# Optimization experiments

Hardware: AMD Instinct MI355X
Metric: run time of the kernel (lower is better)

Reference implementation:

```python
import jax, jax.numpy as jnp
import numpy as np

B, T, E, H = 4, 1024, 1024, 16
F = E // H  # head_feature = 64
EPS = 1e-5


def setup_inputs() -> dict:
    key = jax.random.key(0)
    ks = jax.random.split(key, 7)
    return {
        "x": jax.random.normal(ks[0], (B, T, E), dtype=jnp.float32),
        "q_w": jax.random.normal(ks[1], (H, E, F), dtype=jnp.float32),
        "k_w": jax.random.normal(ks[2], (H, E, F), dtype=jnp.float32),
        "v_w": jax.random.normal(ks[3], (H, E, F), dtype=jnp.float32),
        "fr_w": jax.random.normal(ks[4], (B, E, E), dtype=jnp.float32),
        "ff_w": jax.random.normal(ks[5], (E, E), dtype=jnp.float32),
        "ff_b": jax.random.normal(ks[6], (E,), dtype=jnp.float32),
        "ln1_w": jnp.ones((T, E), dtype=jnp.float32),
        "ln1_b": jnp.zeros((T, E), dtype=jnp.float32),
        "ln2_w": jnp.ones((T, E), dtype=jnp.float32),
        "ln2_b": jnp.zeros((T, E), dtype=jnp.float32),
    }


def _layernorm_2d(x, w, b):
    # LayerNorm over the last TWO dims ([T, E]), matching nn.LayerNorm([T, E])
    mean = jnp.mean(x, axis=(-2, -1), keepdims=True)
    var = jnp.mean(jnp.square(x - mean), axis=(-2, -1), keepdims=True)
    return (x - mean) * jax.lax.rsqrt(var + EPS) * w + b


def _attention(x, q_w, k_w, v_w, fr_w):
    # projections: [B,T,E] x [H,E,F] -> [B,H,T,F]
    q = jnp.einsum("bte,hef->bhtf", x, q_w)
    k = jnp.einsum("bte,hef->bhtf", x, k_w)
    v = jnp.einsum("bte,hef->bhtf", x, v_w)
    scores = jnp.einsum("bhqf,bhkf->bhqk", q, k)  # [B,H,T,T]
    # faithful to source: multiplicative mask (-1e9 on strict upper tri, +1 added everywhere)
    ones = jnp.ones((T, T), dtype=scores.dtype)
    mask = -1.0e9 * jnp.triu(ones, k=1) + ones
    scores = scores * mask
    attn = jax.nn.softmax(scores / jnp.sqrt(jnp.float32(F)), axis=-1)
    z = jnp.einsum("bhqk,bhkf->bhqf", attn, v)  # [B,H,T,F]
    z = z.transpose(0, 2, 1, 3).reshape(B, T, E)  # merge heads
    return jnp.einsum("bte,bed->btd", z, fr_w)  # per-batch feature reduction


def reference(x, q_w, k_w, v_w, fr_w, ff_w, ff_b, ln1_w, ln1_b, ln2_w, ln2_b):
    z = _attention(x, q_w, k_w, v_w, fr_w)
    z1 = _layernorm_2d(x + z, ln1_w, ln1_b)
    z2 = jax.nn.relu(jnp.einsum("bte,de->btd", z1, ff_w) + ff_b)
    return _layernorm_2d(z1 + z2, ln2_w, ln2_b)
```

## Files before the change

### kernel.cpp

```cpp
#include <hip/hip_runtime.h>
#include <math.h>

constexpr int Bc = 4, Tc = 1024, Ec = 1024, Hc = 16, Fc = 64;

typedef __attribute__((ext_vector_type(8))) short bf16x8;
typedef __attribute__((ext_vector_type(4))) float f32x4;

__device__ __forceinline__ ushort f2bf(float x) {
  union { float f; unsigned u; } v; v.f = x;
  unsigned r = v.u + 0x7fffu + ((v.u >> 16) & 1u);
  return (ushort)(r >> 16);
}
__device__ __forceinline__ float bf2f(ushort h) {
  union { float f; unsigned u; } v; v.u = ((unsigned)h) << 16; return v.f;
}
__device__ __forceinline__ void split3(float x, ushort& h, ushort& m, ushort& l) {
  h = f2bf(x);
  float r1 = x - bf2f(h);
  m = f2bf(r1);
  float r2 = r1 - bf2f(m);
  l = f2bf(r2);
}
__device__ __forceinline__ void split2(float x, ushort& h, ushort& l) {
  h = f2bf(x);
  l = f2bf(x - bf2f(h));
}
__device__ __forceinline__ void split3t(float x, ushort& h, ushort& m, ushort& l) {
  union { float f; unsigned u; } v; v.f = x;
  h = (ushort)(v.u >> 16);
  union { float f; unsigned u; } hf; hf.u = v.u & 0xffff0000u;
  float r1 = x - hf.f;
  union { float f; unsigned u; } v1; v1.f = r1;
  m = (ushort)(v1.u >> 16);
  union { float f; unsigned u; } mf; mf.u = v1.u & 0xffff0000u;
  float r2 = r1 - mf.f;
  union { float f; unsigned u; } v2; v2.f = r2;
  l = (ushort)(v2.u >> 16);
}

#define FRAG_IDX(tile, quad, l) (((((tile) * 4) + (quad)) * 16 + (l)) * 8)

__global__ __launch_bounds__(256) void x_split(
    const float* __restrict__ x, ushort* __restrict__ xh,
    ushort* __restrict__ xm, ushort* __restrict__ xl)
{
  const int i = blockIdx.x * 256 + threadIdx.x;
  const float4 a = ((const float4*)x)[i * 2];
  const float4 b = ((const float4*)x)[i * 2 + 1];
  const float xs[8] = {a.x, a.y, a.z, a.w, b.x, b.y, b.z, b.w};
  bf16x8 h, m, l;
#pragma unroll
  for (int j = 0; j < 8; ++j) {
    ushort hu, mu, lu;
    split3t(xs[j], hu, mu, lu);
    h[j] = (short)hu; m[j] = (short)mu; l[j] = (short)lu;
  }
  ((bf16x8*)xh)[i] = h;
  ((bf16x8*)xm)[i] = m;
  ((bf16x8*)xl)[i] = l;
}

__global__ __launch_bounds__(256) void transp_w(
    const float* __restrict__ qw, const float* __restrict__ kw,
    const float* __restrict__ vw, ushort* __restrict__ wT)
{
  const int zi = blockIdx.z;
  const float* src = (zi == 0) ? qw : (zi == 1) ? kw : vw;
  ushort* dst = wT + (size_t)(zi * 3) * (1u << 20);
  const int ns = (zi == 2) ? 1 : 3;
  const int h = blockIdx.y, e0 = blockIdx.x * 64;
  __shared__ float T[64][68];
  const int tid = threadIdx.x;
  {
    const int er = tid >> 4, fr = (tid & 15) * 4;
#pragma unroll
    for (int i = 0; i < 4; ++i) {
      const float4 v = *(const float4*)&src[((size_t)(h * 1024 + e0 + er + i * 16)) * 64 + fr];
      *(float4*)&T[er + i * 16][fr] = v;
    }
  }
  __syncthreads();
  const int f = tid >> 2, eo = (tid & 3) * 16;
  ushort hs[16], ms[16], ls[16];
#pragma unroll
  for (int j = 0; j < 16; ++j) split3(T[eo + j][f], hs[j], ms[j], ls[j]);
  const size_t nbase = (size_t)(h * 64 + f) * 1024 + e0 + eo;
  bf16x8 v0, v1;
#pragma unroll
  for (int j = 0; j < 8; ++j) { v0[j] = (short)hs[j]; v1[j] = (short)hs[j + 8]; }
  *(bf16x8*)&dst[nbase] = v0; *(bf16x8*)&dst[nbase + 8] = v1;
  if (ns == 3) {
#pragma unroll
    for (int j = 0; j < 8; ++j) { v0[j] = (short)ms[j]; v1[j] = (short)ms[j + 8]; }
    *(bf16x8*)&dst[(1u << 20) + nbase] = v0; *(bf16x8*)&dst[(1u << 20) + nbase + 8] = v1;
#pragma unroll
    for (int j = 0; j < 8; ++j) { v0[j] = (short)ls[j]; v1[j] = (short)ls[j + 8]; }
    *(bf16x8*)&dst[(2u << 20) + nbase] = v0; *(bf16x8*)&dst[(2u << 20) + nbase + 8] = v1;
  }
}

__global__ __launch_bounds__(256) void transp_frw(
    const float* __restrict__ frw, ushort* __restrict__ frT)
{
  const int bb = blockIdx.z;
  const int e0 = blockIdx.x * 64, d0 = blockIdx.y * 64;
  __shared__ float T[64][68];
  const int tid = threadIdx.x;
  {
    const int er = tid >> 4, dr = (tid & 15) * 4;
#pragma unroll
    for (int i = 0; i < 4; ++i) {
      const float4 v = *(const float4*)&frw[((size_t)bb * 1024 + e0 + er + i * 16) * 1024 + d0 + dr];
      *(float4*)&T[er + i * 16][dr] = v;
    }
  }
  __syncthreads();
  const int d = tid >> 2, eo = (tid & 3) * 16;
  ushort hs[16], ls[16];
#pragma unroll
  for (int j = 0; j < 16; ++j) split2(T[eo + j][d], hs[j], ls[j]);
  const size_t nbase = ((size_t)bb * 1024 + d0 + d) * 1024 + e0 + eo;
  bf16x8 v0, v1;
#pragma unroll
  for (int j = 0; j < 8; ++j) { v0[j] = (short)hs[j]; v1[j] = (short)hs[j + 8]; }
  *(bf16x8*)&frT[nbase] = v0; *(bf16x8*)&frT[nbase + 8] = v1;
#pragma unroll
  for (int j = 0; j < 8; ++j) { v0[j] = (short)ls[j]; v1[j] = (short)ls[j + 8]; }
  *(bf16x8*)&frT[(4u << 20) + nbase] = v0; *(bf16x8*)&frT[(4u << 20) + nbase + 8] = v1;
}

__global__ __launch_bounds__(256) void proj_all_ps(
    const ushort* __restrict__ xh, const ushort* __restrict__ xm,
    const ushort* __restrict__ xl, const ushort* __restrict__ wT,
    float* __restrict__ qf, ushort* __restrict__ kh,
    ushort* __restrict__ km, ushort* __restrict__ kl,
    ushort* __restrict__ vt)
{
  const int zi = blockIdx.z;
  const int m0 = blockIdx.x * 128, n0 = blockIdx.y * 128;
  __shared__ ushort As[3 * 4096];
  __shared__ ushort Bs[3 * 4096];
  const int tid = threadIdx.x;
  const int wave = tid >> 6, lane = tid & 63, l15 = lane & 15, quad = lane >> 4;
  const int wm = wave >> 1, wn = wave & 1;
  const int sr = tid >> 1, q0 = (tid & 1) * 2;
  const int wb0 = FRAG_IDX(sr >> 4, q0, sr & 15);
  const int wb1 = FRAG_IDX(sr >> 4, q0 + 1, sr & 15);
  f32x4 acc[4][4] = {};

  const size_t arow = (size_t)(m0 + sr) * 1024 + q0 * 8;
  const ushort* axh = xh + arow;
  const ushort* axm = xm + arow;
  const ushort* axl = xl + arow;

  if (zi < 2) {
    const ushort* wt = wT + (size_t)zi * 3 * (1u << 20);
    const ushort* bpb = wt + (size_t)(n0 + sr) * 1024 + q0 * 8;
    bf16x8 pah0 = *(const bf16x8*)(axh);
    bf16x8 pah1 = *(const bf16x8*)(axh + 8);
    bf16x8 pam0 = *(const bf16x8*)(axm);
    bf16x8 pam1 = *(const bf16x8*)(axm + 8);
    bf16x8 pal0 = *(const bf16x8*)(axl);
    bf16x8 pal1 = *(const bf16x8*)(axl + 8);
    bf16x8 pb0[3], pb1[3];
#pragma unroll
    for (int s = 0; s < 3; ++s) {
      const ushort* bp = bpb + ((size_t)s << 20);
      pb0[s] = *(const bf16x8*)(bp);
      pb1[s] = *(const bf16x8*)(bp + 8);
    }
    for (int k0 = 0; k0 < 1024; k0 += 32) {
      __syncthreads();
      {
        *(bf16x8*)&As[wb0] = pah0;        *(bf16x8*)&As[wb1] = pah1;
        *(bf16x8*)&As[4096 + wb0] = pam0; *(bf16x8*)&As[4096 + wb1] = pam1;
        *(bf16x8*)&As[8192 + wb0] = pal0; *(bf16x8*)&As[8192 + wb1] = pal1;
#pragma unroll
        for (int s = 0; s < 3; ++s) {
          *(bf16x8*)&Bs[s * 4096 + wb0] = pb0[s];
          *(bf16x8*)&Bs[s * 4096 + wb1] = pb1[s];
        }
      }
      __syncthreads();
      if (k0 < 992) {
        const int ko = k0 + 32;
        pah0 = *(const bf16x8*)(axh + ko);
        pah1 = *(const bf16x8*)(axh + ko + 8);
        pam0 = *(const bf16x8*)(axm + ko);
        pam1 = *(const bf16x8*)(axm + ko + 8);
        pal0 = *(const bf16x8*)(axl + ko);
        pal1 = *(const bf16x8*)(axl + ko + 8);
#pragma unroll
        for (int s = 0; s < 3; ++s) {
          const ushort* bp = bpb + ((size_t)s << 20) + ko;
          pb0[s] = *(const bf16x8*)(bp);
          pb1[s] = *(const bf16x8*)(bp + 8);
        }
      }
      bf16x8 af[4][3];
#pragma unroll
      for (int tm = 0; tm < 4; ++tm)
#pragma unroll
        for (int s = 0; s < 3; ++s)
          af[tm][s] = *(const bf16x8*)&As[s * 4096 + FRAG_IDX(wm * 4 + tm, quad, l15)];
#pragma unroll
      for (int tn = 0; tn < 4; ++tn) {
        const int bi = FRAG_IDX(wn * 4 + tn, quad, l15);
        bf16x8 b0 = *(const bf16x8*)&Bs[bi];
        bf16x8 b1 = *(const bf16x8*)&Bs[4096 + bi];
        bf16x8 b2 = *(const bf16x8*)&Bs[8192 + bi];
#pragma unroll
        for (int tm = 0; tm < 4; ++tm) {
          f32x4 a = acc[tm][tn];
          a = __builtin_amdgcn_mfma_f32_16x16x32_bf16(af[tm][0], b0, a, 0, 0, 0);
          a = __builtin_amdgcn_mfma_f32_16x16x32_bf16(af[tm][0], b1, a, 0, 0, 0);
          a = __builtin_amdgcn_mfma_f32_16x16x32_bf16(af[tm][1], b0, a, 0, 0, 0);
          a = __builtin_amdgcn_mfma_f32_16x16x32_bf16(af[tm][0], b2, a, 0, 0, 0);
          a = __builtin_amdgcn_mfma_f32_16x16x32_bf16(af[tm][1], b1, a, 0, 0, 0);
          a = __builtin_amdgcn_mfma_f32_16x16x32_bf16(af[tm][2], b0, a, 0, 0, 0);
          acc[tm][tn] = a;
        }
      }
    }
#pragma unroll
    for (int tm = 0; tm < 4; ++tm) {
#pragma unroll
      for (int tn = 0; tn < 4; ++tn) {
#pragma unroll
        for (int r = 0; r < 4; ++r) {
          int m = m0 + wm * 64 + tm * 16 + quad * 4 + r;
          int n = n0 + wn * 64 + tn * 16 + l15;
          int b = m >> 10, t = m & 1023, h = n >> 6, f = n & 63;
          size_t idx = (((size_t)(b * 16 + h)) * 1024 + t) * 64 + f;
          if (zi == 0) {
            qf[idx] = acc[tm][tn][r];
          } else {
            ushort hu, mu, lu;
            split3(acc[tm][tn][r], hu, mu, lu);
            kh[idx] = hu; km[idx] = mu; kl[idx] = lu;
          }
        }
      }
    }
  } else {
    const ushort* wt = wT + (size_t)6 * (1u << 20);
    const ushort* bpb = wt + (size_t)(n0 + sr) * 1024 + q0 * 8;
    bf16x8 pah0 = *(const bf16x8*)(axh);
    bf16x8 pah1 = *(const bf16x8*)(axh + 8);
    bf16x8 pb0 = *(const bf16x8*)(bpb);
    bf16x8 pb1 = *(const bf16x8*)(bpb + 8);
    for (int k0 = 0; k0 < 1024; k0 += 32) {
      __syncthreads();
      {
        *(bf16x8*)&As[wb0] = pah0; *(bf16x8*)&As[wb1] = pah1;
        *(bf16x8*)&Bs[wb0] = pb0;  *(bf16x8*)&Bs[wb1] = pb1;
      }
      __syncthreads();
      if (k0 < 992) {
        const int ko = k0 + 32;
        pah0 = *(const bf16x8*)(axh + ko);
        pah1 = *(const bf16x8*)(axh + ko + 8);
        pb0 = *(const bf16x8*)(bpb + ko);
        pb1 = *(const bf16x8*)(bpb + ko + 8);
      }
      bf16x8 af[4];
#pragma unroll
      for (int tm = 0; tm < 4; ++tm)
        af[tm] = *(const bf16x8*)&As[FRAG_IDX(wm * 4 + tm, quad, l15)];
#pragma unroll
      for (int tn = 0; tn < 4; ++tn) {
        bf16x8 b0 = *(const bf16x8*)&Bs[FRAG_IDX(wn * 4 + tn, quad, l15)];
#pragma unroll
        for (int tm = 0; tm < 4; ++tm)
          acc[tm][tn] = __builtin_amdgcn_mfma_f32_16x16x32_bf16(af[tm], b0, acc[tm][tn], 0, 0, 0);
      }
    }
#pragma unroll
    for (int tm = 0; tm < 4; ++tm) {
#pragma unroll
      for (int tn = 0; tn < 4; ++tn) {
#pragma unroll
        for (int r = 0; r < 4; ++r) {
          int m = m0 + wm * 64 + tm * 16 + quad * 4 + r;
          int n = n0 + wn * 64 + tn * 16 + l15;
          int b = m >> 10, t = m & 1023, h = n >> 6, f = n & 63;
          vt[(((size_t)(b * 16 + h)) * 64 + f) * 1024 + t] = f2bf(acc[tm][tn][r]);
        }
      }
    }
  }
}

__global__ __launch_bounds__(256) void proj_all_mfma(
    const float* __restrict__ x, const ushort* __restrict__ wT,
    float* __restrict__ qf, ushort* __restrict__ kh,
    ushort* __restrict__ km, ushort* __restrict__ kl,
    ushort* __restrict__ vt)
{
  const int zi = blockIdx.z;
  const int m0 = blockIdx.x * 128, n0 = blockIdx.y * 128;
  __shared__ ushort As[3 * 4096];
  __shared__ ushort Bs[3 * 4096];
  const int tid = threadIdx.x;
  const int wave = tid >> 6, lane = tid & 63, l15 = lane & 15, quad = lane >> 4;
  const int wm = wave >> 1, wn = wave & 1;
  const int sr = tid >> 1, q0 = (tid & 1) * 2;
  const int wb0 = FRAG_IDX(sr >> 4, q0, sr & 15);
  const int wb1 = FRAG_IDX(sr >> 4, q0 + 1, sr & 15);
  f32x4 acc[4][4] = {};

  const float* apx = x + (size_t)(m0 + sr) * 1024 + q0 * 8;
  float4 px0 = *(const float4*)(apx);
  float4 px1 = *(const float4*)(apx + 4);
  float4 px2 = *(const float4*)(apx + 8);
  float4 px3 = *(const float4*)(apx + 12);

  if (zi < 2) {
    const ushort* wt = wT + (size_t)zi * 3 * (1u << 20);
    const ushort* bpb = wt + (size_t)(n0 + sr) * 1024 + q0 * 8;
    bf16x8 pb0[3], pb1[3];
#pragma unroll
    for (int s = 0; s < 3; ++s) {
      const ushort* bp = bpb + ((size_t)s << 20);
      pb0[s] = *(const bf16x8*)(bp);
      pb1[s] = *(const bf16x8*)(bp + 8);
    }
    for (int k0 = 0; k0 < 1024; k0 += 32) {
      __syncthreads();
      {
        float xs[16];
        *(float4*)&xs[0]  = px0;
        *(float4*)&xs[4]  = px1;
        *(float4*)&xs[8]  = px2;
        *(float4*)&xs[12] = px3;
        bf16x8 h0, h1, m0v, m1v, l0, l1;
#pragma unroll
        for (int j = 0; j < 8; ++j) {
          ushort hu, mu, lu;
          split3t(xs[j], hu, mu, lu);
          h0[j] = (short)hu; m0v[j] = (short)mu; l0[j] = (short)lu;
          split3t(xs[j + 8], hu, mu, lu);
          h1[j] = (short)hu; m1v[j] = (short)mu; l1[j] = (short)lu;
        }
        *(bf16x8*)&As[wb0] = h0;          *(bf16x8*)&As[wb1] = h1;
        *(bf16x8*)&As[4096 + wb0] = m0v;  *(bf16x8*)&As[4096 + wb1] = m1v;
        *(bf16x8*)&As[8192 + wb0] = l0;   *(bf16x8*)&As[8192 + wb1] = l1;
#pragma unroll
        for (int s = 0; s < 3; ++s) {
          *(bf16x8*)&Bs[s * 4096 + wb0] = pb0[s];
          *(bf16x8*)&Bs[s * 4096 + wb1] = pb1[s];
        }
      }
      __syncthreads();
      if (k0 < 992) {
        const float* nx = apx + k0 + 32;
        px0 = *(const float4*)(nx);
        px1 = *(const float4*)(nx + 4);
        px2 = *(const float4*)(nx + 8);
        px3 = *(const float4*)(nx + 12);
#pragma unroll
        for (int s = 0; s < 3; ++s) {
          const ushort* bp = bpb + ((size_t)s << 20) + k0 + 32;
          pb0[s] = *(const bf16x8*)(bp);
          pb1[s] = *(const bf16x8*)(bp + 8);
        }
      }
      bf16x8 af[4][3];
#pragma unroll
      for (int tm = 0; tm < 4; ++tm)
#pragma unroll
        for (int s = 0; s < 3; ++s)
          af[tm][s] = *(const bf16x8*)&As[s * 4096 + FRAG_IDX(wm * 4 + tm, quad, l15)];
#pragma unroll
      for (int tn = 0; tn < 4; ++tn) {
        const int bi = FRAG_IDX(wn * 4 + tn, quad, l15);
        bf16x8 b0 = *(const bf16x8*)&Bs[bi];
        bf16x8 b1 = *(const bf16x8*)&Bs[4096 + bi];
        bf16x8 b2 = *(const bf16x8*)&Bs[8192 + bi];
#pragma unroll
        for (int tm = 0; tm < 4; ++tm) {
          f32x4 a = acc[tm][tn];
          a = __builtin_amdgcn_mfma_f32_16x16x32_bf16(af[tm][0], b0, a, 0, 0, 0);
          a = __builtin_amdgcn_mfma_f32_16x16x32_bf16(af[tm][0], b1, a, 0, 0, 0);
          a = __builtin_amdgcn_mfma_f32_16x16x32_bf16(af[tm][1], b0, a, 0, 0, 0);
          a = __builtin_amdgcn_mfma_f32_16x16x32_bf16(af[tm][0], b2, a, 0, 0, 0);
          a = __builtin_amdgcn_mfma_f32_16x16x32_bf16(af[tm][1], b1, a, 0, 0, 0);
          a = __builtin_amdgcn_mfma_f32_16x16x32_bf16(af[tm][2], b0, a, 0, 0, 0);
          acc[tm][tn] = a;
        }
      }
    }
#pragma unroll
    for (int tm = 0; tm < 4; ++tm) {
#pragma unroll
      for (int tn = 0; tn < 4; ++tn) {
#pragma unroll
        for (int r = 0; r < 4; ++r) {
          int m = m0 + wm * 64 + tm * 16 + quad * 4 + r;
          int n = n0 + wn * 64 + tn * 16 + l15;
          int b = m >> 10, t = m & 1023, h = n >> 6, f = n & 63;
          size_t idx = (((size_t)(b * 16 + h)) * 1024 + t) * 64 + f;
          if (zi == 0) {
            qf[idx] = acc[tm][tn][r];
          } else {
            ushort hu, mu, lu;
            split3(acc[tm][tn][r], hu, mu, lu);
            kh[idx] = hu; km[idx] = mu; kl[idx] = lu;
          }
        }
      }
    }
  } else {
    const ushort* wt = wT + (size_t)6 * (1u << 20);
    const ushort* bpb = wt + (size_t)(n0 + sr) * 1024 + q0 * 8;
    bf16x8 pb0 = *(const bf16x8*)(bpb);
    bf16x8 pb1 = *(const bf16x8*)(bpb + 8);
    for (int k0 = 0; k0 < 1024; k0 += 32) {
      __syncthreads();
      {
        float xs[16];
        *(float4*)&xs[0]  = px0;
        *(float4*)&xs[4]  = px1;
        *(float4*)&xs[8]  = px2;
        *(float4*)&xs[12] = px3;
        bf16x8 h0, h1;
#pragma unroll
        for (int j = 0; j < 8; ++j) {
          h0[j] = (short)f2bf(xs[j]);
          h1[j] = (short)f2bf(xs[j + 8]);
        }
        *(bf16x8*)&As[wb0] = h0; *(bf16x8*)&As[wb1] = h1;
        *(bf16x8*)&Bs[wb0] = pb0; *(bf16x8*)&Bs[wb1] = pb1;
      }
      __syncthreads();
      if (k0 < 992) {
        const float* nx = apx + k0 + 32;
        px0 = *(const float4*)(nx);
        px1 = *(const float4*)(nx + 4);
        px2 = *(const float4*)(nx + 8);
        px3 = *(const float4*)(nx + 12);
        pb0 = *(const bf16x8*)(bpb + k0 + 32);
        pb1 = *(const bf16x8*)(bpb + k0 + 40);
      }
      bf16x8 af[4];
#pragma unroll
      for (int tm = 0; tm < 4; ++tm)
        af[tm] = *(const bf16x8*)&As[FRAG_IDX(wm * 4 + tm, quad, l15)];
#pragma unroll
      for (int tn = 0; tn < 4; ++tn) {
        bf16x8 b0 = *(const bf16x8*)&Bs[FRAG_IDX(wn * 4 + tn, quad, l15)];
#pragma unroll
        for (int tm = 0; tm < 4; ++tm)
          acc[tm][tn] = __builtin_amdgcn_mfma_f32_16x16x32_bf16(af[tm], b0, acc[tm][tn], 0, 0, 0);
      }
    }
#pragma unroll
    for (int tm = 0; tm < 4; ++tm) {
#pragma unroll
      for (int tn = 0; tn < 4; ++tn) {
#pragma unroll
        for (int r = 0; r < 4; ++r) {
          int m = m0 + wm * 64 + tm * 16 + quad * 4 + r;
          int n = n0 + wn * 64 + tn * 16 + l15;
          int b = m >> 10, t = m & 1023, h = n >> 6, f = n & 63;
          vt[(((size_t)(b * 16 + h)) * 64 + f) * 1024 + t] = f2bf(acc[tm][tn][r]);
        }
      }
    }
  }
}

__global__ __launch_bounds__(512) void attn_mfma(
    const float* __restrict__ qf, const ushort* __restrict__ kh,
    const ushort* __restrict__ km, const ushort* __restrict__ kl,
    const ushort* __restrict__ vt, ushort* __restrict__ zh, ushort* __restrict__ zl)
{
  __shared__ ushort Ks[3][64][68];
  __shared__ ushort Vs[64][68];
  __shared__ ushort Pl[8][16][68];

  const int tid = threadIdx.x;
  const int wave = tid >> 6, lane = tid & 63;
  const int l15 = lane & 15, quad = lane >> 4;
  const int bh = blockIdx.y;
  const int qbase = blockIdx.x * 128;

  bf16x8 aqh[2], aqm[2], aql[2];
  {
    const int qrow = qbase + wave * 16 + l15;
    const float* qp = qf + ((size_t)bh * Tc + qrow) * Fc;
#pragma unroll
    for (int ks = 0; ks < 2; ++ks) {
      int f0 = ks * 32 + quad * 8;
      float4 x0 = *(const float4*)(qp + f0);
      float4 x1 = *(const float4*)(qp + f0 + 4);
      float xs[8] = {x0.x, x0.y, x0.z, x0.w, x1.x, x1.y, x1.z, x1.w};
#pragma unroll
      for (int j = 0; j < 8; ++j) {
        ushort hu, mu, lu;
        split3(xs[j], hu, mu, lu);
        aqh[ks][j] = (short)hu; aqm[ks][j] = (short)mu; aql[ks][j] = (short)lu;
      }
    }
  }

  f32x4 o[4] = {{0,0,0,0},{0,0,0,0},{0,0,0,0},{0,0,0,0}};
  float m_run[4], l_run[4];
#pragma unroll
  for (int r = 0; r < 4; ++r) { m_run[r] = -1e30f; l_run[r] = 0.f; }

  const int srow = tid >> 3, sc8 = tid & 7;
  const size_t kbase = (size_t)bh * Tc * Fc;
  const size_t vbase = (size_t)bh * Fc * Tc;
  const ushort* kp0 = kh + kbase + (size_t)srow * Fc + sc8 * 8;
  const ushort* kp1 = km + kbase + (size_t)srow * Fc + sc8 * 8;
  const ushort* kp2 = kl + kbase + (size_t)srow * Fc + sc8 * 8;
  const ushort* vp  = vt + vbase + (size_t)srow * Tc + sc8 * 8;

  for (int kt = 0; kt < Tc; kt += 64) {
    __syncthreads();
    {
      const size_t ko = (size_t)kt * Fc;
      *(bf16x8*)&Ks[0][srow][sc8 * 8] = *(const bf16x8*)(kp0 + ko);
      *(bf16x8*)&Ks[1][srow][sc8 * 8] = *(const bf16x8*)(kp1 + ko);
      *(bf16x8*)&Ks[2][srow][sc8 * 8] = *(const bf16x8*)(kp2 + ko);
      *(bf16x8*)&Vs[srow][sc8 * 8]    = *(const bf16x8*)(vp + kt);
    }
    __syncthreads();

    f32x4 sacc[4] = {{0,0,0,0},{0,0,0,0},{0,0,0,0},{0,0,0,0}};
#pragma unroll
    for (int nt = 0; nt < 4; ++nt) {
      int key = nt * 16 + l15;
#pragma unroll
      for (int ks = 0; ks < 2; ++ks) {
        int f0 = ks * 32 + quad * 8;
        bf16x8 bh_ = *(const bf16x8*)&Ks[0][key][f0];
        bf16x8 bm_ = *(const bf16x8*)&Ks[1][key][f0];
        bf16x8 bl_ = *(const bf16x8*)&Ks[2][key][f0];
        sacc[nt] = __builtin_amdgcn_mfma_f32_16x16x32_bf16(aqh[ks], bh_, sacc[nt], 0, 0, 0);
        sacc[nt] = __builtin_amdgcn_mfma_f32_16x16x32_bf16(aqh[ks], bm_, sacc[nt], 0, 0, 0);
        sacc[nt] = __builtin_amdgcn_mfma_f32_16x16x32_bf16(aqm[ks], bh_, sacc[nt], 0, 0, 0);
        sacc[nt] = __builtin_amdgcn_mfma_f32_16x16x32_bf16(aqh[ks], bl_, sacc[nt], 0, 0, 0);
        sacc[nt] = __builtin_amdgcn_mfma_f32_16x16x32_bf16(aqm[ks], bm_, sacc[nt], 0, 0, 0);
        sacc[nt] = __builtin_amdgcn_mfma_f32_16x16x32_bf16(aql[ks], bh_, sacc[nt], 0, 0, 0);
      }
    }

    const int rowg0 = qbase + wave * 16 + quad * 4;
    float mx[4];
#pragma unroll
    for (int r = 0; r < 4; ++r) mx[r] = -1e30f;
#pragma unroll
    for (int nt = 0; nt < 4; ++nt) {
      int key = kt + nt * 16 + l15;
#pragma unroll
      for (int r = 0; r < 4; ++r) {
        float s = sacc[nt][r];
        if (key > rowg0 + r) s *= -1.0e9f + 1.0f;
        s *= 0.125f;
        sacc[nt][r] = s;
        mx[r] = fmaxf(mx[r], s);
      }
    }
#pragma unroll
    for (int r = 0; r < 4; ++r)
#pragma unroll
      for (int d = 1; d < 16; d <<= 1) mx[r] = fmaxf(mx[r], __shfl_xor(mx[r], d));

    float corr[4], ps[4];
#pragma unroll
    for (int r = 0; r < 4; ++r) {
      float m2 = fmaxf(m_run[r], mx[r]);
      corr[r] = __expf(m_run[r] - m2);
      m_run[r] = m2;
      ps[r] = 0.f;
    }
#pragma unroll
    for (int nt = 0; nt < 4; ++nt) {
#pragma unroll
      for (int r = 0; r < 4; ++r) {
        float p = __expf(sacc[nt][r] - m_run[r]);
        ps[r] += p;
        Pl[wave][quad * 4 + r][nt * 16 + l15] = f2bf(p);
      }
    }
#pragma unroll
    for (int r = 0; r < 4; ++r) {
#pragma unroll
      for (int d = 1; d < 16; d <<= 1) ps[r] += __shfl_xor(ps[r], d);
      l_run[r] = l_run[r] * corr[r] + ps[r];
#pragma unroll
      for (int ft = 0; ft < 4; ++ft) o[ft][r] *= corr[r];
    }

#pragma unroll
    for (int ks2 = 0; ks2 < 2; ++ks2) {
      bf16x8 pa = *(const bf16x8*)&Pl[wave][l15][ks2 * 32 + quad * 8];
#pragma unroll
      for (int ft = 0; ft < 4; ++ft) {
        bf16x8 vb = *(const bf16x8*)&Vs[ft * 16 + l15][ks2 * 32 + quad * 8];
        o[ft] = __builtin_amdgcn_mfma_f32_16x16x32_bf16(pa, vb, o[ft], 0, 0, 0);
      }
    }
  }

  const int b = bh >> 4, h = bh & 15;
#pragma unroll
  for (int r = 0; r < 4; ++r) {
    float inv = 1.f / l_run[r];
    int row = qbase + wave * 16 + quad * 4 + r;
    size_t base = ((size_t)(b * Tc + row)) * Ec + h * Fc;
#pragma unroll
    for (int ft = 0; ft < 4; ++ft) {
      ushort hu, lu;
      split2(o[ft][r] * inv, hu, lu);
      zh[base + ft * 16 + l15] = hu;
      zl[base + ft * 16 + l15] = lu;
    }
  }
}

__global__ __launch_bounds__(256) void gemm_fr_mfma(
    const ushort* __restrict__ zh, const ushort* __restrict__ zl,
    const ushort* __restrict__ frT, const float* __restrict__ x,
    float* __restrict__ s1, float2* __restrict__ part)
{
  const int bb = blockIdx.z;
  const int m0 = blockIdx.x * 128, n0 = blockIdx.y * 64;
  __shared__ ushort Ah[4096], Al[4096], Bh[2048], Bl[2048];
  __shared__ float2 red[256];
  const int tid = threadIdx.x;
  const int wave = tid >> 6, lane = tid & 63, l15 = lane & 15, quad = lane >> 4;
  const int wm = wave >> 1, wn = wave & 1;
  const int sr = tid >> 1, q0 = (tid & 1) * 2;
  const int wb0 = FRAG_IDX(sr >> 4, q0, sr & 15);
  const int wb1 = FRAG_IDX(sr >> 4, q0 + 1, sr & 15);
  const int sr2 = tid >> 2, qb = tid & 3;
  const int wbB = FRAG_IDX(sr2 >> 4, qb, sr2 & 15);
  f32x4 acc[4][2] = {};
  const size_t abase = ((size_t)bb * 1024 + m0 + sr) * 1024 + q0 * 8;
  const size_t bbase = ((size_t)bb * 1024 + n0 + sr2) * 1024 + qb * 8;
  const ushort* blp = frT + (4u << 20);
  bf16x8 pAh0 = *(const bf16x8*)(zh + abase);
  bf16x8 pAh1 = *(const bf16x8*)(zh + abase + 8);
  bf16x8 pAl0 = *(const bf16x8*)(zl + abase);
  bf16x8 pAl1 = *(const bf16x8*)(zl + abase + 8);
  bf16x8 pBh  = *(const bf16x8*)(frT + bbase);
  bf16x8 pBl  = *(const bf16x8*)(blp + bbase);
  for (int k0 = 0; k0 < 1024; k0 += 32) {
    __syncthreads();
    {
      *(bf16x8*)&Ah[wb0] = pAh0;
      *(bf16x8*)&Ah[wb1] = pAh1;
      *(bf16x8*)&Al[wb0] = pAl0;
      *(bf16x8*)&Al[wb1] = pAl1;
      *(bf16x8*)&Bh[wbB] = pBh;
      *(bf16x8*)&Bl[wbB] = pBl;
    }
    __syncthreads();
    if (k0 < 992) {
      pAh0 = *(const bf16x8*)(zh + abase + k0 + 32);
      pAh1 = *(const bf16x8*)(zh + abase + k0 + 40);
      pAl0 = *(const bf16x8*)(zl + abase + k0 + 32);
      pAl1 = *(const bf16x8*)(zl + abase + k0 + 40);
      pBh  = *(const bf16x8*)(frT + bbase + k0 + 32);
      pBl  = *(const bf16x8*)(blp + bbase + k0 + 32);
    }
    bf16x8 ah[4], al[4];
#pragma unroll
    for (int tm = 0; tm < 4; ++tm) {
      ah[tm] = *(const bf16x8*)&Ah[FRAG_IDX(wm * 4 + tm, quad, l15)];
      al[tm] = *(const bf16x8*)&Al[FRAG_IDX(wm * 4 + tm, quad, l15)];
    }
#pragma unroll
    for (int tn = 0; tn < 2; ++tn) {
      const int bi = FRAG_IDX(wn * 2 + tn, quad, l15);
      bf16x8 b0 = *(const bf16x8*)&Bh[bi];
      bf16x8 b1 = *(const bf16x8*)&Bl[bi];
#pragma unroll
      for (int tm = 0; tm < 4; ++tm) {
        f32x4 a = acc[tm][tn];
        a = __builtin_amdgcn_mfma_f32_16x16x32_bf16(ah[tm], b0, a, 0, 0, 0);
        a = __builtin_amdgcn_mfma_f32_16x16x32_bf16(ah[tm], b1, a, 0, 0, 0);
        a = __builtin_amdgcn_mfma_f32_16x16x32_bf16(al[tm], b0, a, 0, 0, 0);
        acc[tm][tn] = a;
      }
    }
  }
  float sum = 0.f, sq = 0.f;
#pragma unroll
  for (int tm = 0; tm < 4; ++tm) {
#pragma unroll
    for (int tn = 0; tn < 2; ++tn) {
#pragma unroll
      for (int r = 0; r < 4; ++r) {
        int m = m0 + wm * 64 + tm * 16 + quad * 4 + r;
        int n = n0 + wn * 32 + tn * 16 + l15;
        size_t idx = ((size_t)bb * 1024 + m) * 1024 + n;
        float o = x[idx] + acc[tm][tn][r];
        s1[idx] = o;
        sum += o; sq += o * o;
      }
    }
  }
  red[tid] = make_float2(sum, sq);
  __syncthreads();
  for (int s = 128; s > 0; s >>= 1) {
    if (tid < s) { red[tid].x += red[tid + s].x; red[tid].y += red[tid + s].y; }
    __syncthreads();
  }
  if (tid == 0) part[bb * 128 + blockIdx.x * 16 + blockIdx.y] = red[0];
}

__global__ __launch_bounds__(256) void gemm_ff_mfma(
    const ushort* __restrict__ z1h, const ushort* __restrict__ z1l,
    const ushort* __restrict__ fwh, const ushort* __restrict__ fwl,
    const float* __restrict__ ffb, float* __restrict__ s2,
    float2* __restrict__ part)
{
  const int m0 = blockIdx.x * 128, n0 = blockIdx.y * 64;
  __shared__ ushort Ah[4096], Al[4096], Bh[2048], Bl[2048];
  __shared__ float2 red[256];
  const int tid = threadIdx.x;
  const int wave = tid >> 6, lane = tid & 63, l15 = lane & 15, quad = lane >> 4;
  const int wm = wave >> 1, wn = wave & 1;
  const int sr = tid >> 1, q0 = (tid & 1) * 2;
  const int wb0 = FRAG_IDX(sr >> 4, q0, sr & 15);
  const int wb1 = FRAG_IDX(sr >> 4, q0 + 1, sr & 15);
  const int sr2 = tid >> 2, qb = tid & 3;
  const int wbB = FRAG_IDX(sr2 >> 4, qb, sr2 & 15);
  f32x4 acc[4][2] = {};
  const size_t abase = (size_t)(m0 + sr) * 1024 + q0 * 8;
  const size_t bbase = (size_t)(n0 + sr2) * 1024 + qb * 8;
  bf16x8 pAh0 = *(const bf16x8*)(z1h + abase);
  bf16x8 pAh1 = *(const bf16x8*)(z1h + abase + 8);
  bf16x8 pAl0 = *(const bf16x8*)(z1l + abase);
  bf16x8 pAl1 = *(const bf16x8*)(z1l + abase + 8);
  bf16x8 pBh  = *(const bf16x8*)(fwh + bbase);
  bf16x8 pBl  = *(const bf16x8*)(fwl + bbase);
  for (int k0 = 0; k0 < 1024; k0 += 32) {
    __syncthreads();
    {
      *(bf16x8*)&Ah[wb0] = pAh0;
      *(bf16x8*)&Ah[wb1] = pAh1;
      *(bf16x8*)&Al[wb0] = pAl0;
      *(bf16x8*)&Al[wb1] = pAl1;
      *(bf16x8*)&Bh[wbB] = pBh;
      *(bf16x8*)&Bl[wbB] = pBl;
    }
    __syncthreads();
    if (k0 < 992) {
      pAh0 = *(const bf16x8*)(z1h + abase + k0 + 32);
      pAh1 = *(const bf16x8*)(z1h + abase + k0 + 40);
      pAl0 = *(const bf16x8*)(z1l + abase + k0 + 32);
      pAl1 = *(const bf16x8*)(z1l + abase + k0 + 40);
      pBh  = *(const bf16x8*)(fwh + bbase + k0 + 32);
      pBl  = *(const bf16x8*)(fwl + bbase + k0 + 32);
    }
    bf16x8 ah[4], al[4];
#pragma unroll
    for (int tm = 0; tm < 4; ++tm) {
      ah[tm] = *(const bf16x8*)&Ah[FRAG_IDX(wm * 4 + tm, quad, l15)];
      al[tm] = *(const bf16x8*)&Al[FRAG_IDX(wm * 4 + tm, quad, l15)];
    }
#pragma unroll
    for (int tn = 0; tn < 2; ++tn) {
      const int bi = FRAG_IDX(wn * 2 + tn, quad, l15);
      bf16x8 b0 = *(const bf16x8*)&Bh[bi];
      bf16x8 b1 = *(const bf16x8*)&Bl[bi];
#pragma unroll
      for (int tm = 0; tm < 4; ++tm) {
        f32x4 a = acc[tm][tn];
        a = __builtin_amdgcn_mfma_f32_16x16x32_bf16(ah[tm], b0, a, 0, 0, 0);
        a = __builtin_amdgcn_mfma_f32_16x16x32_bf16(ah[tm], b1, a, 0, 0, 0);
        a = __builtin_amdgcn_mfma_f32_16x16x32_bf16(al[tm], b0, a, 0, 0, 0);
        acc[tm][tn] = a;
      }
    }
  }
  float sum = 0.f, sq = 0.f;
#pragma unroll
  for (int tm = 0; tm < 4; ++tm) {
#pragma unroll
    for (int tn = 0; tn < 2; ++tn) {
#pragma unroll
      for (int r = 0; r < 4; ++r) {
        int m = m0 + wm * 64 + tm * 16 + quad * 4 + r;
        int n = n0 + wn * 32 + tn * 16 + l15;
        size_t idx = (size_t)m * 1024 + n;
        float z1v = bf2f(z1h[idx]) + bf2f(z1l[idx]);
        float o = z1v + fmaxf(acc[tm][tn][r] + ffb[n], 0.f);
        s2[idx] = o;
        sum += o; sq += o * o;
      }
    }
  }
  red[tid] = make_float2(sum, sq);
  __syncthreads();
  for (int s = 128; s > 0; s >>= 1) {
    if (tid < s) { red[tid].x += red[tid + s].x; red[tid].y += red[tid + s].y; }
    __syncthreads();
  }
  if (tid == 0) part[blockIdx.x * 16 + blockIdx.y] = red[0];
}

__global__ __launch_bounds__(256) void ln_stats(
    const float2* __restrict__ part, float2* __restrict__ stats, int npart)
{
  __shared__ double sd[256], sq[256];
  const int tid = threadIdx.x;
  double as = 0.0, aq = 0.0;
  for (int i = tid; i < npart; i += 256) {
    float2 p = part[blockIdx.x * npart + i];
    as += (double)p.x; aq += (double)p.y;
  }
  sd[tid] = as; sq[tid] = aq;
  __syncthreads();
  for (int s = 128; s > 0; s >>= 1) {
    if (tid < s) { sd[tid] += sd[tid + s]; sq[tid] += sq[tid + s]; }
    __syncthreads();
  }
  if (tid == 0) {
    const double n = (double)Tc * Ec;
    double mean = sd[0] / n;
    double var = sq[0] / n - mean * mean;
    if (var < 0.0) var = 0.0;
    double rs = 1.0 / sqrt(var + 1e-5);
    stats[blockIdx.x] = make_float2((float)mean, (float)rs);
  }
}

__global__ __launch_bounds__(256) void ln_norm_split(
    const float* __restrict__ s, const float2* __restrict__ stats,
    const float* __restrict__ w, const float* __restrict__ bias,
    ushort* __restrict__ oh, ushort* __restrict__ ol,
    const float* __restrict__ ffw, ushort* __restrict__ fwh, ushort* __restrict__ fwl)
{
  if (blockIdx.x >= 4096) {
    int i = (blockIdx.x - 4096) * 256 + threadIdx.x;
#pragma unroll
    for (int j = 0; j < 4; ++j) {
      int idx = i * 4 + j;
      float4 v = ((const float4*)ffw)[idx];
      ushort4 h, l;
      split2(v.x, h.x, l.x); split2(v.y, h.y, l.y);
      split2(v.z, h.z, l.z); split2(v.w, h.w, l.w);
      ((ushort4*)fwh)[idx] = h; ((ushort4*)fwl)[idx] = l;
    }
    return;
  }
  int i = blockIdx.x * 256 + threadIdx.x;
  int b = i >> 18;
  int te4 = i & ((1 << 18) - 1);
  float2 st = stats[b];
  float4 sv = ((const float4*)s)[i];
  float4 wv = ((const float4*)w)[te4];
  float4 bv = ((const float4*)bias)[te4];
  float4 o;
  o.x = (sv.x - st.x) * st.y * wv.x + bv.x;
  o.y = (sv.y - st.x) * st.y * wv.y + bv.y;
  o.z = (sv.z - st.x) * st.y * wv.z + bv.z;
  o.w = (sv.w - st.x) * st.y * wv.w + bv.w;
  ushort4 h, l;
  split2(o.x, h.x, l.x); split2(o.y, h.y, l.y);
  split2(o.z, h.z, l.z); split2(o.w, h.w, l.w);
  ((ushort4*)oh)[i] = h; ((ushort4*)ol)[i] = l;
}

__global__ __launch_bounds__(256) void ln_norm(
    const float* __restrict__ s, const float2* __restrict__ stats,
    const float* __restrict__ w, const float* __restrict__ bias,
    float* __restrict__ out)
{
  int i = blockIdx.x * 256 + threadIdx.x;
  if (i >= (Bc * Tc * Ec) / 4) return;
  int b = i >> 18;
  int te4 = i & ((1 << 18) - 1);
  float2 st = stats[b];
  float4 sv = ((const float4*)s)[i];
  float4 wv = ((const float4*)w)[te4];
  float4 bv = ((const float4*)bias)[te4];
  float4 o;
  o.x = (sv.x - st.x) * st.y * wv.x + bv.x;
  o.y = (sv.y - st.x) * st.y * wv.y + bv.y;
  o.z = (sv.z - st.x) * st.y * wv.z + bv.z;
  o.w = (sv.w - st.x) * st.y * wv.w + bv.w;
  ((float4*)out)[i] = o;
}

extern "C" void kernel_launch(void* const* d_in, const int* in_sizes, int n_in,
                              void* d_out, int out_size, void* d_ws, size_t ws_size,
                              hipStream_t stream)
{
  const float* x    = (const float*)d_in[0];
  const float* qw   = (const float*)d_in[1];
  const float* kw   = (const float*)d_in[2];
  const float* vw   = (const float*)d_in[3];
  const float* frw  = (const float*)d_in[4];
  const float* ffw  = (const float*)d_in[5];
  const float* ffb  = (const float*)d_in[6];
  const float* ln1w = (const float*)d_in[7];
  const float* ln1b = (const float*)d_in[8];
  const float* ln2w = (const float*)d_in[9];
  const float* ln2b = (const float*)d_in[10];
  float* out = (float*)d_out;
  char* W = (char*)d_ws;

  const size_t MB = 1ull << 20;
  float*  qf  = (float*)(W);
  ushort* kh  = (ushort*)(W + 16 * MB);
  ushort* km  = (ushort*)(W + 24 * MB);
  ushort* kl  = (ushort*)(W + 32 * MB);
  ushort* vt  = (ushort*)(W + 40 * MB);
  ushort* wT  = (ushort*)(W + 48 * MB);
  ushort* zh  = (ushort*)(W + 48 * MB);
  ushort* zl  = (ushort*)(W + 56 * MB);
  ushort* frT = (ushort*)(W + 16 * MB);
  float*  s1  = (float*)(W);
  ushort* z1h = (ushort*)(W + 16 * MB);
  ushort* z1l = (ushort*)(W + 24 * MB);
  ushort* fwh = (ushort*)(W + 48 * MB);
  ushort* fwl = (ushort*)(W + 50 * MB);
  float*  s2  = (float*)(W + 32 * MB);
  float2* part1  = (float2*)(W + 64 * MB);
  float2* part2  = part1 + 1024;
  float2* stats1 = part2 + 1024;
  float2* stats2 = stats1 + 4;
  ushort* xh = (ushort*)(W + 65 * MB);
  ushort* xm = (ushort*)(W + 73 * MB);
  ushort* xl = (ushort*)(W + 81 * MB);
  const bool big_ws = ws_size >= 90 * MB;

  transp_w<<<dim3(16, 16, 3), 256, 0, stream>>>(qw, kw, vw, wT);
  if (big_ws) {
    x_split<<<dim3(2048), 256, 0, stream>>>(x, xh, xm, xl);
    proj_all_ps<<<dim3(32, 8, 3), 256, 0, stream>>>(xh, xm, xl, wT, qf, kh, km, kl, vt);
  } else {
    proj_all_mfma<<<dim3(32, 8, 3), 256, 0, stream>>>(x, wT, qf, kh, km, kl, vt);
  }
  attn_mfma<<<dim3(8, 64), 512, 0, stream>>>(qf, kh, km, kl, vt, zh, zl);
  transp_frw<<<dim3(16, 16, 4), 256, 0, stream>>>(frw, frT);
  gemm_fr_mfma<<<dim3(8, 16, 4), 256, 0, stream>>>(zh, zl, frT, x, s1, part1);
  ln_stats<<<dim3(4), 256, 0, stream>>>(part1, stats1, 128);
  ln_norm_split<<<dim3(4352), 256, 0, stream>>>(s1, stats1, ln1w, ln1b, z1h, z1l,
                                                ffw, fwh, fwl);
  gemm_ff_mfma<<<dim3(32, 16), 256, 0, stream>>>(z1h, z1l, fwh, fwl, ffb, s2, part2);
  ln_stats<<<dim3(4), 256, 0, stream>>>(part2, stats2, 128);
  ln_norm<<<dim3(4096), 256, 0, stream>>>(s2, stats2, ln2w, ln2b, out);
}
```

Baseline: 412.2 us.

## Merge weight transpose and x split into one launch; remap GEMM tile loads

Fuses the q/k/v weight transpose-split kernel and the x split kernel into one launch, so one kernel launch and a serialization point go away. In the projection, feature-reduction and feed-forward GEMMs, each thread now loads rows matching its lane/quad fragment position, which makes the shared-memory stores contiguous (lane*8) rather than scattered FRAG_IDX writes. The global loads become 16-byte segments strided across rows per lane, which may coalesce worse in exchange for conflict-free LDS writes.

```diff
diff --git a/kernel.cpp b/kernel.cpp
--- a/kernel.cpp
+++ b/kernel.cpp
@@ -40,37 +40,37 @@
 
 #define FRAG_IDX(tile, quad, l) (((((tile) * 4) + (quad)) * 16 + (l)) * 8)
 
-__global__ __launch_bounds__(256) void x_split(
+__global__ __launch_bounds__(256) void prep_all(
+    const float* __restrict__ qw, const float* __restrict__ kw,
+    const float* __restrict__ vw, ushort* __restrict__ wT,
     const float* __restrict__ x, ushort* __restrict__ xh,
     ushort* __restrict__ xm, ushort* __restrict__ xl)
 {
-  const int i = blockIdx.x * 256 + threadIdx.x;
-  const float4 a = ((const float4*)x)[i * 2];
-  const float4 b = ((const float4*)x)[i * 2 + 1];
-  const float xs[8] = {a.x, a.y, a.z, a.w, b.x, b.y, b.z, b.w};
-  bf16x8 h, m, l;
-#pragma unroll
-  for (int j = 0; j < 8; ++j) {
-    ushort hu, mu, lu;
-    split3t(xs[j], hu, mu, lu);
-    h[j] = (short)hu; m[j] = (short)mu; l[j] = (short)lu;
-  }
-  ((bf16x8*)xh)[i] = h;
-  ((bf16x8*)xm)[i] = m;
-  ((bf16x8*)xl)[i] = l;
-}
-
-__global__ __launch_bounds__(256) void transp_w(
-    const float* __restrict__ qw, const float* __restrict__ kw,
-    const float* __restrict__ vw, ushort* __restrict__ wT)
-{
   const int zi = blockIdx.z;
+  const int tid = threadIdx.x;
+  if (zi >= 3) {
+    const int bid = (zi - 3) * 256 + blockIdx.y * 16 + blockIdx.x;
+    const int i = bid * 256 + tid;
+    const float4 a = ((const float4*)x)[i * 2];
+    const float4 b = ((const float4*)x)[i * 2 + 1];
+    const float xs[8] = {a.x, a.y, a.z, a.w, b.x, b.y, b.z, b.w};
+    bf16x8 h, m, l;
+#pragma unroll
+    for (int j = 0; j < 8; ++j) {
+      ushort hu, mu, lu;
+      split3t(xs[j], hu, mu, lu);
+      h[j] = (short)hu; m[j] = (short)mu; l[j] = (short)lu;
+    }
+    ((bf16x8*)xh)[i] = h;
+    ((bf16x8*)xm)[i] = m;
+    ((bf16x8*)xl)[i] = l;
+    return;
+  }
   const float* src = (zi == 0) ? qw : (zi == 1) ? kw : vw;
   ushort* dst = wT + (size_t)(zi * 3) * (1u << 20);
   const int ns = (zi == 2) ? 1 : 3;
   const int h = blockIdx.y, e0 = blockIdx.x * 64;
   __shared__ float T[64][68];
-  const int tid = threadIdx.x;
   {
     const int er = tid >> 4, fr = (tid & 15) * 4;
 #pragma unroll
@@ -143,58 +143,58 @@
   const int tid = threadIdx.x;
   const int wave = tid >> 6, lane = tid & 63, l15 = lane & 15, quad = lane >> 4;
   const int wm = wave >> 1, wn = wave & 1;
-  const int sr = tid >> 1, q0 = (tid & 1) * 2;
-  const int wb0 = FRAG_IDX(sr >> 4, q0, sr & 15);
-  const int wb1 = FRAG_IDX(sr >> 4, q0 + 1, sr & 15);
+  const int ac1 = (wave * 64 + lane) * 8, ac2 = ac1 + 2048;
   f32x4 acc[4][4] = {};
 
-  const size_t arow = (size_t)(m0 + sr) * 1024 + q0 * 8;
-  const ushort* axh = xh + arow;
-  const ushort* axm = xm + arow;
-  const ushort* axl = xl + arow;
+  const size_t arow1 = (size_t)(m0 + wave * 16 + l15) * 1024 + quad * 8;
+  const size_t arow2 = arow1 + (size_t)64 * 1024;
+  const ushort* axh1 = xh + arow1; const ushort* axh2 = xh + arow2;
+  const ushort* axm1 = xm + arow1; const ushort* axm2 = xm + arow2;
+  const ushort* axl1 = xl + arow1; const ushort* axl2 = xl + arow2;
 
   if (zi < 2) {
     const ushort* wt = wT + (size_t)zi * 3 * (1u << 20);
-    const ushort* bpb = wt + (size_t)(n0 + sr) * 1024 + q0 * 8;
-    bf16x8 pah0 = *(const bf16x8*)(axh);
-    bf16x8 pah1 = *(const bf16x8*)(axh + 8);
-    bf16x8 pam0 = *(const bf16x8*)(axm);
-    bf16x8 pam1 = *(const bf16x8*)(axm + 8);
-    bf16x8 pal0 = *(const bf16x8*)(axl);
-    bf16x8 pal1 = *(const bf16x8*)(axl + 8);
+    const size_t brow1 = (size_t)(n0 + wave * 16 + l15) * 1024 + quad * 8;
+    const size_t brow2 = brow1 + (size_t)64 * 1024;
+    bf16x8 pah0 = *(const bf16x8*)(axh1);
+    bf16x8 pah1 = *(const bf16x8*)(axh2);
+    bf16x8 pam0 = *(const bf16x8*)(axm1);
+    bf16x8 pam1 = *(const bf16x8*)(axm2);
+    bf16x8 pal0 = *(const bf16x8*)(axl1);
+    bf16x8 pal1 = *(const bf16x8*)(axl2);
     bf16x8 pb0[3], pb1[3];
 #pragma unroll
     for (int s = 0; s < 3; ++s) {
-      const ushort* bp = bpb + ((size_t)s << 20);
-      pb0[s] = *(const bf16x8*)(bp);
-      pb1[s] = *(const bf16x8*)(bp + 8);
+      const ushort* bp = wt + ((size_t)s << 20);
+      pb0[s] = *(const bf16x8*)(bp + brow1);
+      pb1[s] = *(const bf16x8*)(bp + brow2);
     }
     for (int k0 = 0; k0 < 1024; k0 += 32) {
       __syncthreads();
       {
-        *(bf16x8*)&As[wb0] = pah0;        *(bf16x8*)&As[wb1] = pah1;
-        *(bf16x8*)&As[4096 + wb0] = pam0; *(bf16x8*)&As[4096 + wb1] = pam1;
-        *(bf16x8*)&As[8192 + wb0] = pal0; *(bf16x8*)&As[8192 + wb1] = pal1;
+        *(bf16x8*)&As[ac1] = pah0;        *(bf16x8*)&As[ac2] = pah1;
+        *(bf16x8*)&As[4096 + ac1] = pam0; *(bf16x8*)&As[4096 + ac2] = pam1;
+        *(bf16x8*)&As[8192 + ac1] = pal0; *(bf16x8*)&As[8192 + ac2] = pal1;
 #pragma unroll
         for (int s = 0; s < 3; ++s) {
-          *(bf16x8*)&Bs[s * 4096 + wb0] = pb0[s];
-          *(bf16x8*)&Bs[s * 4096 + wb1] = pb1[s];
+          *(bf16x8*)&Bs[s * 4096 + ac1] = pb0[s];
+          *(bf16x8*)&Bs[s * 4096 + ac2] = pb1[s];
         }
       }
       __syncthreads();
       if (k0 < 992) {
         const int ko = k0 + 32;
-        pah0 = *(const bf16x8*)(axh + ko);
-        pah1 = *(const bf16x8*)(axh + ko + 8);
-        pam0 = *(const bf16x8*)(axm + ko);
-        pam1 = *(const bf16x8*)(axm + ko + 8);
-        pal0 = *(const bf16x8*)(axl + ko);
-        pal1 = *(const bf16x8*)(axl + ko + 8);
+        pah0 = *(const bf16x8*)(axh1 + ko);
+        pah1 = *(const bf16x8*)(axh2 + ko);
+        pam0 = *(const bf16x8*)(axm1 + ko);
+        pam1 = *(const bf16x8*)(axm2 + ko);
+        pal0 = *(const bf16x8*)(axl1 + ko);
+        pal1 = *(const bf16x8*)(axl2 + ko);
 #pragma unroll
         for (int s = 0; s < 3; ++s) {
-          const ushort* bp = bpb + ((size_t)s << 20) + ko;
-          pb0[s] = *(const bf16x8*)(bp);
-          pb1[s] = *(const bf16x8*)(bp + 8);
+          const ushort* bp = wt + ((size_t)s << 20) + ko;
+          pb0[s] = *(const bf16x8*)(bp + brow1);
+          pb1[s] = *(const bf16x8*)(bp + brow2);
         }
       }
       bf16x8 af[4][3];
@@ -244,24 +244,25 @@
     }
   } else {
     const ushort* wt = wT + (size_t)6 * (1u << 20);
-    const ushort* bpb = wt + (size_t)(n0 + sr) * 1024 + q0 * 8;
-    bf16x8 pah0 = *(const bf16x8*)(axh);
-    bf16x8 pah1 = *(const bf16x8*)(axh + 8);
-    bf16x8 pb0 = *(const bf16x8*)(bpb);
-    bf16x8 pb1 = *(const bf16x8*)(bpb + 8);
+    const size_t brow1 = (size_t)(n0 + wave * 16 + l15) * 1024 + quad * 8;
+    const size_t brow2 = brow1 + (size_t)64 * 1024;
+    bf16x8 pah0 = *(const bf16x8*)(axh1);
+    bf16x8 pah1 = *(const bf16x8*)(axh2);
+    bf16x8 pb0 = *(const bf16x8*)(wt + brow1);
+    bf16x8 pb1 = *(const bf16x8*)(wt + brow2);
     for (int k0 = 0; k0 < 1024; k0 += 32) {
       __syncthreads();
       {
-        *(bf16x8*)&As[wb0] = pah0; *(bf16x8*)&As[wb1] = pah1;
-        *(bf16x8*)&Bs[wb0] = pb0;  *(bf16x8*)&Bs[wb1] = pb1;
+        *(bf16x8*)&As[ac1] = pah0; *(bf16x8*)&As[ac2] = pah1;
+        *(bf16x8*)&Bs[ac1] = pb0;  *(bf16x8*)&Bs[ac2] = pb1;
       }
       __syncthreads();
       if (k0 < 992) {
         const int ko = k0 + 32;
-        pah0 = *(const bf16x8*)(axh + ko);
-        pah1 = *(const bf16x8*)(axh + ko + 8);
-        pb0 = *(const bf16x8*)(bpb + ko);
-        pb1 = *(const bf16x8*)(bpb + ko + 8);
+        pah0 = *(const bf16x8*)(axh1 + ko);
+        pah1 = *(const bf16x8*)(axh2 + ko);
+        pb0 = *(const bf16x8*)(wt + brow1 + ko);
+        pb1 = *(const bf16x8*)(wt + brow2 + ko);
       }
       bf16x8 af[4];
 #pragma unroll
@@ -633,37 +634,34 @@
   const int tid = threadIdx.x;
   const int wave = tid >> 6, lane = tid & 63, l15 = lane & 15, quad = lane >> 4;
   const int wm = wave >> 1, wn = wave & 1;
-  const int sr = tid >> 1, q0 = (tid & 1) * 2;
-  const int wb0 = FRAG_IDX(sr >> 4, q0, sr & 15);
-  const int wb1 = FRAG_IDX(sr >> 4, q0 + 1, sr & 15);
-  const int sr2 = tid >> 2, qb = tid & 3;
-  const int wbB = FRAG_IDX(sr2 >> 4, qb, sr2 & 15);
+  const int ac1 = (wave * 64 + lane) * 8, ac2 = ac1 + 2048;
   f32x4 acc[4][2] = {};
-  const size_t abase = ((size_t)bb * 1024 + m0 + sr) * 1024 + q0 * 8;
-  const size_t bbase = ((size_t)bb * 1024 + n0 + sr2) * 1024 + qb * 8;
+  const size_t abase1 = ((size_t)bb * 1024 + m0 + wave * 16 + l15) * 1024 + quad * 8;
+  const size_t abase2 = abase1 + (size_t)64 * 1024;
+  const size_t bbase = ((size_t)bb * 1024 + n0 + wave * 16 + l15) * 1024 + quad * 8;
   const ushort* blp = frT + (4u << 20);
-  bf16x8 pAh0 = *(const bf16x8*)(zh + abase);
-  bf16x8 pAh1 = *(const bf16x8*)(zh + abase + 8);
-  bf16x8 pAl0 = *(const bf16x8*)(zl + abase);
-  bf16x8 pAl1 = *(const bf16x8*)(zl + abase + 8);
+  bf16x8 pAh0 = *(const bf16x8*)(zh + abase1);
+  bf16x8 pAh1 = *(const bf16x8*)(zh + abase2);
+  bf16x8 pAl0 = *(const bf16x8*)(zl + abase1);
+  bf16x8 pAl1 = *(const bf16x8*)(zl + abase2);
   bf16x8 pBh  = *(const bf16x8*)(frT + bbase);
   bf16x8 pBl  = *(const bf16x8*)(blp + bbase);
   for (int k0 = 0; k0 < 1024; k0 += 32) {
     __syncthreads();
     {
-      *(bf16x8*)&Ah[wb0] = pAh0;
-      *(bf16x8*)&Ah[wb1] = pAh1;
-      *(bf16x8*)&Al[wb0] = pAl0;
-      *(bf16x8*)&Al[wb1] = pAl1;
-      *(bf16x8*)&Bh[wbB] = pBh;
-      *(bf16x8*)&Bl[wbB] = pBl;
+      *(bf16x8*)&Ah[ac1] = pAh0;
+      *(bf16x8*)&Ah[ac2] = pAh1;
+      *(bf16x8*)&Al[ac1] = pAl0;
+      *(bf16x8*)&Al[ac2] = pAl1;
+      *(bf16x8*)&Bh[ac1] = pBh;
+      *(bf16x8*)&Bl[ac1] = pBl;
     }
     __syncthreads();
     if (k0 < 992) {
-      pAh0 = *(const bf16x8*)(zh + abase + k0 + 32);
-      pAh1 = *(const bf16x8*)(zh + abase + k0 + 40);
-      pAl0 = *(const bf16x8*)(zl + abase + k0 + 32);
-      pAl1 = *(const bf16x8*)(zl + abase + k0 + 40);
+      pAh0 = *(const bf16x8*)(zh + abase1 + k0 + 32);
+      pAh1 = *(const bf16x8*)(zh + abase2 + k0 + 32);
+      pAl0 = *(const bf16x8*)(zl + abase1 + k0 + 32);
+      pAl1 = *(const bf16x8*)(zl + abase2 + k0 + 32);
       pBh  = *(const bf16x8*)(frT + bbase + k0 + 32);
       pBl  = *(const bf16x8*)(blp + bbase + k0 + 32);
     }
@@ -725,36 +723,33 @@
   const int tid = threadIdx.x;
   const int wave = tid >> 6, lane = tid & 63, l15 = lane & 15, quad = lane >> 4;
   const int wm = wave >> 1, wn = wave & 1;
-  const int sr = tid >> 1, q0 = (tid & 1) * 2;
-  const int wb0 = FRAG_IDX(sr >> 4, q0, sr & 15);
-  const int wb1 = FRAG_IDX(sr >> 4, q0 + 1, sr & 15);
-  const int sr2 = tid >> 2, qb = tid & 3;
-  const int wbB = FRAG_IDX(sr2 >> 4, qb, sr2 & 15);
+  const int ac1 = (wave * 64 + lane) * 8, ac2 = ac1 + 2048;
   f32x4 acc[4][2] = {};
-  const size_t abase = (size_t)(m0 + sr) * 1024 + q0 * 8;
-  const size_t bbase = (size_t)(n0 + sr2) * 1024 + qb * 8;
-  bf16x8 pAh0 = *(const bf16x8*)(z1h + abase);
-  bf16x8 pAh1 = *(const bf16x8*)(z1h + abase + 8);
-  bf16x8 pAl0 = *(const bf16x8*)(z1l + abase);
-  bf16x8 pAl1 = *(const bf16x8*)(z1l + abase + 8);
+  const size_t abase1 = (size_t)(m0 + wave * 16 + l15) * 1024 + quad * 8;
+  const size_t abase2 = abase1 + (size_t)64 * 1024;
+  const size_t bbase = (size_t)(n0 + wave * 16 + l15) * 1024 + quad * 8;
+  bf16x8 pAh0 = *(const bf16x8*)(z1h + abase1);
+  bf16x8 pAh1 = *(const bf16x8*)(z1h + abase2);
+  bf16x8 pAl0 = *(const bf16x8*)(z1l + abase1);
+  bf16x8 pAl1 = *(const bf16x8*)(z1l + abase2);
   bf16x8 pBh  = *(const bf16x8*)(fwh + bbase);
   bf16x8 pBl  = *(const bf16x8*)(fwl + bbase);
   for (int k0 = 0; k0 < 1024; k0 += 32) {
     __syncthreads();
     {
-      *(bf16x8*)&Ah[wb0] = pAh0;
-      *(bf16x8*)&Ah[wb1] = pAh1;
-      *(bf16x8*)&Al[wb0] = pAl0;
-      *(bf16x8*)&Al[wb1] = pAl1;
-      *(bf16x8*)&Bh[wbB] = pBh;
-      *(bf16x8*)&Bl[wbB] = pBl;
+      *(bf16x8*)&Ah[ac1] = pAh0;
+      *(bf16x8*)&Ah[ac2] = pAh1;
+      *(bf16x8*)&Al[ac1] = pAl0;
+      *(bf16x8*)&Al[ac2] = pAl1;
+      *(bf16x8*)&Bh[ac1] = pBh;
+      *(bf16x8*)&Bl[ac1] = pBl;
     }
     __syncthreads();
     if (k0 < 992) {
-      pAh0 = *(const bf16x8*)(z1h + abase + k0 + 32);
-      pAh1 = *(const bf16x8*)(z1h + abase + k0 + 40);
-      pAl0 = *(const bf16x8*)(z1l + abase + k0 + 32);
-      pAl1 = *(const bf16x8*)(z1l + abase + k0 + 40);
+      pAh0 = *(const bf16x8*)(z1h + abase1 + k0 + 32);
+      pAh1 = *(const bf16x8*)(z1h + abase2 + k0 + 32);
+      pAl0 = *(const bf16x8*)(z1l + abase1 + k0 + 32);
+      pAl1 = *(const bf16x8*)(z1l + abase2 + k0 + 32);
       pBh  = *(const bf16x8*)(fwh + bbase + k0 + 32);
       pBl  = *(const bf16x8*)(fwl + bbase + k0 + 32);
     }
@@ -932,11 +927,11 @@
   ushort* xl = (ushort*)(W + 81 * MB);
   const bool big_ws = ws_size >= 90 * MB;
 
-  transp_w<<<dim3(16, 16, 3), 256, 0, stream>>>(qw, kw, vw, wT);
   if (big_ws) {
-    x_split<<<dim3(2048), 256, 0, stream>>>(x, xh, xm, xl);
+    prep_all<<<dim3(16, 16, 11), 256, 0, stream>>>(qw, kw, vw, wT, x, xh, xm, xl);
     proj_all_ps<<<dim3(32, 8, 3), 256, 0, stream>>>(xh, xm, xl, wT, qf, kh, km, kl, vt);
   } else {
+    prep_all<<<dim3(16, 16, 3), 256, 0, stream>>>(qw, kw, vw, wT, x, xh, xm, xl);
     proj_all_mfma<<<dim3(32, 8, 3), 256, 0, stream>>>(x, wT, qf, kh, km, kl, vt);
   }
   attn_mfma<<<dim3(8, 64), 512, 0, stream>>>(qf, kh, km, kl, vt, zh, zl);
```

After: 451.7 us. 9.6% more time.
